# Kernel tuning notes

Hardware: AMD Instinct MI355X
Metric: run time of the kernel (lower is better)

## Reference

```python
import jax, jax.numpy as jnp
import numpy as np

B, T, E, D, A = 32, 2048, 1024, 1024, 1024
SHARPENING = 1.0


def setup_inputs() -> dict:
    key = jax.random.key(0)
    ks = jax.random.split(key, 8)
    s = 0.02
    return {
        "enc_out": jax.random.normal(ks[0], (B, T, E), jnp.float32),
        "x_lens": jax.random.randint(ks[1], (B,), 1, T + 1, jnp.int32),
        "dec_out": jax.random.normal(ks[2], (B, 1, D), jnp.float32),
        "att_weights_step": jax.random.uniform(ks[3], (B, T), jnp.float32),
        "W_enc": jax.random.normal(ks[4], (E, A), jnp.float32) * s,
        "b_enc": jnp.zeros((A,), jnp.float32),
        "W_dec": jax.random.normal(ks[5], (D, A), jnp.float32) * s,
        "v": jax.random.normal(ks[6], (A,), jnp.float32) * s,
    }


def reference(enc_out, x_lens, dec_out, att_weights_step, W_enc, b_enc, W_dec, v):
    # content (Bahdanau additive) attention
    # energy[b,t] = v . tanh(W_enc enc[b,t] + b_enc + W_dec dec[b])
    enc_proj = jnp.einsum("bte,ea->bta", enc_out, W_enc) + b_enc  # [B,T,A]
    dec_proj = jnp.einsum("bod,da->boa", dec_out, W_dec)          # [B,1,A]
    energy = jnp.einsum("bta,a->bt", jnp.tanh(enc_proj + dec_proj), v)  # [B,T]
    # original multiplies energy by a 0/1 length mask (NOT -inf masking)
    mask = (jnp.arange(T)[None, :] < x_lens[:, None]).astype(energy.dtype)
    energy = energy * mask * SHARPENING
    att = jax.nn.softmax(energy, axis=-1)  # [B,T]
    context_vec = jnp.einsum("bte,bt->be", enc_out, att)[:, None, :]  # [B,1,E]
    return context_vec, att
```

## Files before the change

### kernel.cpp

```cpp
#include <hip/hip_runtime.h>
#include <hip/hip_bf16.h>
#include <stdint.h>


typedef __bf16 bf16;
typedef __bf16 bf16x8 __attribute__((ext_vector_type(8)));
typedef __bf16 bf16x4 __attribute__((ext_vector_type(4)));
typedef float floatx4 __attribute__((ext_vector_type(4)));

#define T_DIM 2048
#define B_DIM 32
#define K_DIM 1024
#define N_DIM 1024
#define M_DIM (B_DIM * T_DIM)
#define ENC_ELEMS ((size_t)M_DIM * K_DIM)

__device__ __forceinline__ void async_copy16(const bf16* g, bf16* l) {
    __builtin_amdgcn_global_load_lds(
        (const __attribute__((address_space(1))) void*)g,
        (__attribute__((address_space(3))) void*)l, 16, 0, 0);
}

__device__ __forceinline__ float fast_tanh(float x) {
    float ax = fabsf(x);
    float e  = __expf(ax + ax);
    float t  = 1.f - 2.f / (e + 1.f);
    return copysignf(t, x);
}

__global__ __launch_bounds__(256) void cvt_enc(const float* __restrict__ in,
                                               bf16* __restrict__ out) {
    size_t i = ((size_t)blockIdx.x * 256 + threadIdx.x) * 8;
    const size_t stride = (size_t)gridDim.x * 256 * 8;
    for (; i < ENC_ELEMS; i += stride) {
        float4 f0 = *(const float4*)(in + i);
        float4 f1 = *(const float4*)(in + i + 4);
        bf16x8 w;
        w[0] = (bf16)f0.x; w[1] = (bf16)f0.y; w[2] = (bf16)f0.z; w[3] = (bf16)f0.w;
        w[4] = (bf16)f1.x; w[5] = (bf16)f1.y; w[6] = (bf16)f1.z; w[7] = (bf16)f1.w;
        *(bf16x8*)(out + i) = w;
    }
}

__global__ __launch_bounds__(256) void transpose_wenc(
        const float* __restrict__ W, bf16* __restrict__ WT) {
    __shared__ bf16 tile[64][65];
    const int e0 = blockIdx.x * 64, a0 = blockIdx.y * 64;
    const int c = threadIdx.x & 63, r0 = threadIdx.x >> 6;
#pragma unroll
    for (int p = 0; p < 16; ++p) {
        int r = p * 4 + r0;
        tile[r][c] = (bf16)W[(size_t)(e0 + r) * 1024 + a0 + c];
    }
    __syncthreads();
#pragma unroll
    for (int p = 0; p < 16; ++p) {
        int r = p * 4 + r0;
        WT[(size_t)(a0 + r) * 1024 + e0 + c] = tile[c][r];
    }
}

__global__ __launch_bounds__(256) void decproj_kernel(
        const float* __restrict__ dec, const float* __restrict__ Wdec,
        const float* __restrict__ benc, float* __restrict__ dproj) {
    const int bg = blockIdx.x;
    const int y  = blockIdx.y;
    const int a  = y * 256 + threadIdx.x;
    __shared__ float sdec[8][1024];
    for (int i = threadIdx.x; i < 8 * 1024; i += 256)
        sdec[i >> 10][i & 1023] = dec[bg * 8192 + i];
    __syncthreads();
    float acc[8];
    const float be = benc[a];
#pragma unroll
    for (int b = 0; b < 8; ++b) acc[b] = be;
    for (int d = 0; d < 1024; ++d) {
        const float w = Wdec[(size_t)d * 1024 + a];
#pragma unroll
        for (int b = 0; b < 8; ++b) acc[b] += sdec[b][d] * w;
    }
#pragma unroll
    for (int b = 0; b < 8; ++b) dproj[(bg * 8 + b) * 1024 + a] = acc[b];
}


#define HT 8192

#define BARRIER()  asm volatile("s_barrier" ::: "memory")
#define VMCNT(n)   asm volatile("s_waitcnt vmcnt(" #n ")" ::: "memory")

#define STAGE_A(kt, h) {                                                       \
    const bf16* g_ = encb + (size_t)(m0 + (h)*128 + wave*8 + (lane>>3)) * 1024 \
                     + (kt)*64 + srccol;                                       \
    bf16* l_ = As + ((((kt)&1)*2 + (h)) * HT) + wave * 512;                    \
    async_copy16(g_, l_);                                                      \
    async_copy16(g_ + (size_t)64*1024, l_ + 4096);                             \
}
#define STAGE_B(kt, h) {                                                       \
    const bf16* g_ = WT + (size_t)(n0 + (h)*128 + wave*8 + (lane>>3)) * 1024   \
                     + (kt)*64 + srccol;                                       \
    bf16* l_ = Bs + ((((kt)&1)*2 + (h)) * HT) + wave * 512;                    \
    async_copy16(g_, l_);                                                      \
    async_copy16(g_ + (size_t)64*1024, l_ + 4096);                             \
}

#define PHASE(tt, qm, qn, RA, STAGECODE, WAITCODE) {                           \
    const bf16* Ah_ = As + (((tt)&1)*2 + (qm)) * HT;                           \
    const bf16* Bh_ = Bs + (((tt)&1)*2 + (qn)) * HT;                           \
    if (RA) {                                                                  \
      _Pragma("unroll") for (int mf_ = 0; mf_ < 4; ++mf_) {                    \
        afr[mf_][0] = *(const bf16x8*)(Ah_ + (wm*64 + mf_*16 + lo)*64 + swz0); \
        afr[mf_][1] = *(const bf16x8*)(Ah_ + (wm*64 + mf_*16 + lo)*64 + swz1); \
      }                                                                        \
    }                                                                          \
    _Pragma("unroll") for (int nf_ = 0; nf_ < 2; ++nf_) {                      \
      bfr[nf_][0] = *(const bf16x8*)(Bh_ + (wn*32 + nf_*16 + lo)*64 + swz0);   \
      bfr[nf_][1] = *(const bf16x8*)(Bh_ + (wn*32 + nf_*16 + lo)*64 + swz1);   \
    }                                                                          \
    STAGECODE;                                                                 \
    BARRIER();                                                                 \
    __builtin_amdgcn_s_setprio(1);                                             \
    _Pragma("unroll") for (int kk_ = 0; kk_ < 2; ++kk_)                        \
      _Pragma("unroll") for (int mf_ = 0; mf_ < 4; ++mf_)                      \
        _Pragma("unroll") for (int nf_ = 0; nf_ < 2; ++nf_)                    \
          acc[qm][qn][mf_][nf_] = __builtin_amdgcn_mfma_f32_16x16x32_bf16(     \
              afr[mf_][kk_], bfr[nf_][kk_], acc[qm][qn][mf_][nf_], 0, 0, 0);   \
    __builtin_amdgcn_s_setprio(0);                                             \
    WAITCODE;                                                                  \
    BARRIER();                                                                 \
}

__global__ __launch_bounds__(512, 2) void energy_gemm_8ph(
        const bf16* __restrict__ encb, const bf16* __restrict__ WT,
        const float* __restrict__ dproj, const float* __restrict__ v,
        float* __restrict__ part) {
    __shared__ __align__(16) bf16 As[4 * HT];
    __shared__ __align__(16) bf16 Bs[4 * HT];

    const int tid  = threadIdx.x;
    const int lane = tid & 63;
    const int wave = tid >> 6;
    const int wm   = wave >> 2;
    const int wn   = wave & 3;
    const int lo   = lane & 15;
    const int hi   = lane >> 4;

    const int L = blockIdx.x;
    const int xcd  = L & 7;
    const int slot = L >> 3;
    const int m_tile  = xcd * 32 + (slot >> 2);
    const int n_chunk = slot & 3;
    const int m0 = m_tile * 256;
    const int n0 = n_chunk * 256;
    const int b  = m0 >> 11;

    const int srccol = (((lane & 7) ^ (lane >> 3)) << 3);
    const int swz0 = ((hi)     ^ (lo & 7)) << 3;
    const int swz1 = ((4 | hi) ^ (lo & 7)) << 3;

    floatx4 acc[2][2][4][2];
#pragma unroll
    for (int a_ = 0; a_ < 2; ++a_)
#pragma unroll
      for (int b_ = 0; b_ < 2; ++b_)
#pragma unroll
        for (int c_ = 0; c_ < 4; ++c_)
#pragma unroll
          for (int d_ = 0; d_ < 2; ++d_)
            acc[a_][b_][c_][d_] = (floatx4){0.f, 0.f, 0.f, 0.f};

    bf16x8 afr[4][2], bfr[2][2];

    STAGE_A(0, 0); STAGE_B(0, 0); STAGE_A(0, 1); STAGE_B(0, 1);
    STAGE_A(1, 0); STAGE_B(1, 0);
    VMCNT(4);
    BARRIER();

#pragma unroll 1
    for (int i = 0; i < 7; ++i) {
        const int t0 = 2 * i, t1 = 2 * i + 1, t2 = 2 * i + 2, t3 = 2 * i + 3;
        PHASE(t0, 0, 0, 1, { STAGE_A(t1, 1); }, {});
        PHASE(t0, 0, 1, 0, { STAGE_B(t1, 1); }, {});
        PHASE(t0, 1, 0, 1, { STAGE_A(t2, 0); }, {});
        PHASE(t0, 1, 1, 0, { STAGE_B(t2, 0); }, { VMCNT(4); });
        PHASE(t1, 0, 0, 1, { STAGE_A(t2, 1); }, {});
        PHASE(t1, 0, 1, 0, { STAGE_B(t2, 1); }, {});
        PHASE(t1, 1, 0, 1, { STAGE_A(t3, 0); }, {});
        PHASE(t1, 1, 1, 0, { STAGE_B(t3, 0); }, { VMCNT(4); });
    }
    PHASE(14, 0, 0, 1, { STAGE_A(15, 1); }, {});
    PHASE(14, 0, 1, 0, { STAGE_B(15, 1); }, {});
    PHASE(14, 1, 0, 1, {}, {});
    PHASE(14, 1, 1, 0, {}, { VMCNT(0); });
    PHASE(15, 0, 0, 1, {}, {});
    PHASE(15, 0, 1, 0, {}, {});
    PHASE(15, 1, 0, 1, {}, {});
    PHASE(15, 1, 1, 0, {}, {});

    float* esump = (float*)As;

    float vv[2][2], dp[2][2];
#pragma unroll
    for (int qn = 0; qn < 2; ++qn)
#pragma unroll
      for (int nf = 0; nf < 2; ++nf) {
        int col = n0 + qn * 128 + wn * 32 + nf * 16 + lo;
        vv[qn][nf] = v[col];
        dp[qn][nf] = dproj[b * 1024 + col];
      }
#pragma unroll
    for (int qm = 0; qm < 2; ++qm)
#pragma unroll
      for (int mf = 0; mf < 4; ++mf)
#pragma unroll
        for (int r = 0; r < 4; ++r) {
          float s = 0.f;
#pragma unroll
          for (int qn = 0; qn < 2; ++qn)
#pragma unroll
            for (int nf = 0; nf < 2; ++nf)
              s += vv[qn][nf] * fast_tanh(acc[qm][qn][mf][nf][r] + dp[qn][nf]);
          s += __shfl_xor(s, 1);
          s += __shfl_xor(s, 2);
          s += __shfl_xor(s, 4);
          s += __shfl_xor(s, 8);
          if (lo == 0)
            esump[wn * 256 + qm * 128 + wm * 64 + mf * 16 + hi * 4 + r] = s;
        }
    __syncthreads();
    if (tid < 256) {
        float s = esump[tid] + esump[256 + tid] + esump[512 + tid] + esump[768 + tid];
        part[(size_t)n_chunk * M_DIM + m0 + tid] = s;
    }
}

__global__ __launch_bounds__(256) void energy_gemm_f32(
        const float* __restrict__ enc, const bf16* __restrict__ WT,
        const float* __restrict__ dproj, const float* __restrict__ v,
        float* __restrict__ part) {
    __shared__ __align__(16) bf16 As[128 * 32];
    __shared__ __align__(16) bf16 Bs[128 * 32];
    __shared__ float esum[128];

    const int tid  = threadIdx.x;
    const int lane = tid & 63;
    const int wave = tid >> 6;
    const int wy = wave >> 1, wx = wave & 1;
    const int L = blockIdx.x;
    const int xcd  = L & 7;
    const int slot = L >> 3;
    const int m_tile = xcd * 64 + (slot >> 3);
    const int n_chunk = slot & 7;
    const int m0 = m_tile * 128;
    const int n0 = n_chunk * 128;
    const int b  = m0 >> 11;

    if (tid < 128) esum[tid] = 0.f;

    floatx4 acc[4][4];
#pragma unroll
    for (int i = 0; i < 4; ++i)
#pragma unroll
        for (int j = 0; j < 4; ++j) acc[i][j] = (floatx4){0.f, 0.f, 0.f, 0.f};

    const int sr = tid >> 2;
    const int sc = (tid & 3) * 8;
    const float* gA = enc + (size_t)(m0 + sr) * 1024 + sc;
    const bf16*  gB = WT  + (size_t)(n0 + sr) * 1024 + sc;
    bf16* lA = As + sr * 32 + sc;
    bf16* lB = Bs + sr * 32 + sc;

    for (int k0 = 0; k0 < K_DIM; k0 += 32) {
        __syncthreads();
#pragma unroll
        for (int rep = 0; rep < 2; ++rep) {
            const float4* p = (const float4*)(gA + (size_t)rep * 64 * 1024 + k0);
            float4 f0 = p[0], f1 = p[1];
            bf16x8 w;
            w[0] = (bf16)f0.x; w[1] = (bf16)f0.y; w[2] = (bf16)f0.z; w[3] = (bf16)f0.w;
            w[4] = (bf16)f1.x; w[5] = (bf16)f1.y; w[6] = (bf16)f1.z; w[7] = (bf16)f1.w;
            *(bf16x8*)(lA + rep * 64 * 32) = w;
            *(bf16x8*)(lB + rep * 64 * 32) =
                *(const bf16x8*)(gB + (size_t)rep * 64 * 1024 + k0);
        }
        __syncthreads();

        bf16x8 af[4], bfrg[4];
#pragma unroll
        for (int i = 0; i < 4; ++i)
            af[i] = *(const bf16x8*)(As + (wy * 64 + i * 16 + (lane & 15)) * 32 + (lane >> 4) * 8);
#pragma unroll
        for (int i = 0; i < 4; ++i)
            bfrg[i] = *(const bf16x8*)(Bs + (wx * 64 + i * 16 + (lane & 15)) * 32 + (lane >> 4) * 8);
#pragma unroll
        for (int mi = 0; mi < 4; ++mi)
#pragma unroll
            for (int ni = 0; ni < 4; ++ni)
                acc[mi][ni] = __builtin_amdgcn_mfma_f32_16x16x32_bf16(
                    af[mi], bfrg[ni], acc[mi][ni], 0, 0, 0);
    }
    __syncthreads();

    float vv[4], dp[4];
#pragma unroll
    for (int ni = 0; ni < 4; ++ni) {
        int col = n0 + wx * 64 + ni * 16 + (lane & 15);
        vv[ni] = v[col];
        dp[ni] = dproj[b * 1024 + col];
    }
#pragma unroll
    for (int mi = 0; mi < 4; ++mi) {
#pragma unroll
        for (int r = 0; r < 4; ++r) {
            float s = 0.f;
#pragma unroll
            for (int ni = 0; ni < 4; ++ni)
                s += vv[ni] * fast_tanh(acc[mi][ni][r] + dp[ni]);
            s += __shfl_xor(s, 1);
            s += __shfl_xor(s, 2);
            s += __shfl_xor(s, 4);
            s += __shfl_xor(s, 8);
            if ((lane & 15) == 0) {
                int row = wy * 64 + mi * 16 + (lane >> 4) * 4 + r;
                atomicAdd(&esum[row], s);
            }
        }
    }
    __syncthreads();
    if (tid < 128) part[(size_t)n_chunk * M_DIM + m0 + tid] = esum[tid];
}

__global__ __launch_bounds__(256) void softmax_kernel(
        const float* __restrict__ part, const int* __restrict__ xlens,
        float* __restrict__ att, int nc) {
    const int b = blockIdx.x, tid = threadIdx.x;
    const int len = xlens[b];
    float e[8];
    float mx = -3.4e38f;
#pragma unroll
    for (int i = 0; i < 8; ++i) {
        const int t = tid + i * 256;
        float s = 0.f;
#pragma unroll 4
        for (int c = 0; c < nc; ++c) s += part[(size_t)c * M_DIM + b * 2048 + t];
        e[i] = (t < len) ? s : 0.f;
        mx = fmaxf(mx, e[i]);
    }
#pragma unroll
    for (int off = 1; off < 64; off <<= 1) mx = fmaxf(mx, __shfl_xor(mx, off));
    __shared__ float sr1[4], sr2[4];
    if ((tid & 63) == 0) sr1[tid >> 6] = mx;
    __syncthreads();
    mx = fmaxf(fmaxf(sr1[0], sr1[1]), fmaxf(sr1[2], sr1[3]));
    float sum = 0.f;
#pragma unroll
    for (int i = 0; i < 8; ++i) { e[i] = __expf(e[i] - mx); sum += e[i]; }
#pragma unroll
    for (int off = 1; off < 64; off <<= 1) sum += __shfl_xor(sum, off);
    if ((tid & 63) == 0) sr2[tid >> 6] = sum;
    __syncthreads();
    sum = sr2[0] + sr2[1] + sr2[2] + sr2[3];
    const float inv = 1.f / sum;
#pragma unroll
    for (int i = 0; i < 8; ++i)
        att[b * 2048 + tid + i * 256] = e[i] * inv;
}

__global__ __launch_bounds__(256) void context_part_kernel(
        const bf16* __restrict__ encb, const float* __restrict__ att,
        float* __restrict__ ctxpart) {
    const int b = blockIdx.x, chunk = blockIdx.y, tid = threadIdx.x;
    const int t0 = chunk * 128;
    __shared__ float satt[128];
    if (tid < 128) satt[tid] = att[b * 2048 + t0 + tid];
    __syncthreads();
    const bf16* base = encb + ((size_t)b * 2048 + t0) * 1024 + tid * 4;
    float a0 = 0.f, a1 = 0.f, a2 = 0.f, a3 = 0.f;
#pragma unroll 4
    for (int t = 0; t < 128; ++t) {
        bf16x4 ev = *(const bf16x4*)(base + (size_t)t * 1024);
        float w = satt[t];
        a0 += w * (float)ev[0]; a1 += w * (float)ev[1];
        a2 += w * (float)ev[2]; a3 += w * (float)ev[3];
    }
    float* o = ctxpart + ((size_t)b * 16 + chunk) * 1024 + tid * 4;
    o[0] = a0; o[1] = a1; o[2] = a2; o[3] = a3;
}

__global__ __launch_bounds__(256) void context_reduce_kernel(
        const float* __restrict__ ctxpart, float* __restrict__ out_ctx) {
    const int i = blockIdx.x * 256 + threadIdx.x;
    const int b = i >> 10, e = i & 1023;
    const float* p = ctxpart + (size_t)b * 16 * 1024 + e;
    float s = 0.f;
#pragma unroll
    for (int c = 0; c < 16; ++c) s += p[c * 1024];
    out_ctx[i] = s;
}

__global__ __launch_bounds__(256) void context_kernel_f32(
        const float* __restrict__ enc, const float* __restrict__ att,
        float* __restrict__ ctx) {
    const int b = blockIdx.x, t0 = blockIdx.y * 128, tid = threadIdx.x;
    __shared__ float satt[128];
    if (tid < 128) satt[tid] = att[b * 2048 + t0 + tid];
    __syncthreads();
    const float* base = enc + ((size_t)b * 2048 + t0) * 1024 + tid * 4;
    float a0 = 0.f, a1 = 0.f, a2 = 0.f, a3 = 0.f;
    for (int t = 0; t < 128; ++t) {
        float4 ev = *(const float4*)(base + (size_t)t * 1024);
        float w = satt[t];
        a0 += w * ev.x; a1 += w * ev.y; a2 += w * ev.z; a3 += w * ev.w;
    }
    float* o = ctx + b * 1024 + tid * 4;
    atomicAdd(o + 0, a0); atomicAdd(o + 1, a1);
    atomicAdd(o + 2, a2); atomicAdd(o + 3, a3);
}

extern "C" void kernel_launch(void* const* d_in, const int* in_sizes, int n_in,
                              void* d_out, int out_size, void* d_ws, size_t ws_size,
                              hipStream_t stream) {
    const float* enc   = (const float*)d_in[0];
    const int*   xlens = (const int*)d_in[1];
    const float* dec   = (const float*)d_in[2];
    const float* Wenc  = (const float*)d_in[4];
    const float* benc  = (const float*)d_in[5];
    const float* Wdec  = (const float*)d_in[6];
    const float* v     = (const float*)d_in[7];

    float* out_ctx = (float*)d_out;
    float* out_att = out_ctx + B_DIM * K_DIM;

    char* ws = (char*)d_ws;
    float* dproj   = (float*)ws;
    bf16*  WT      = (bf16*)(ws + (128u << 10));
    float* part    = (float*)(ws + (128u << 10) + (2u << 20));
    bf16*  encb    = (bf16*)(ws + (128u << 10) + (4u << 20));
    float* ctxpart = (float*)(ws + (128u << 10) + (4u << 20) + (ENC_ELEMS * 2));
    const size_t need = (128u << 10) + (4u << 20) + ENC_ELEMS * 2 + (2u << 21);

    transpose_wenc<<<dim3(16, 16), 256, 0, stream>>>(Wenc, WT);
    decproj_kernel<<<dim3(4, 4), 256, 0, stream>>>(dec, Wdec, benc, dproj);

    if (ws_size >= need) {
        cvt_enc<<<2048, 256, 0, stream>>>(enc, encb);
        energy_gemm_8ph<<<1024, 512, 0, stream>>>(encb, WT, dproj, v, part);
        softmax_kernel<<<B_DIM, 256, 0, stream>>>(part, xlens, out_att, 4);
        context_part_kernel<<<dim3(B_DIM, 16), 256, 0, stream>>>(encb, out_att, ctxpart);
        context_reduce_kernel<<<B_DIM * K_DIM / 256, 256, 0, stream>>>(ctxpart, out_ctx);
    } else {
        hipMemsetAsync(out_ctx, 0, B_DIM * K_DIM * sizeof(float), stream);
        energy_gemm_f32<<<4096, 256, 0, stream>>>(enc, WT, dproj, v, part);
        softmax_kernel<<<B_DIM, 256, 0, stream>>>(part, xlens, out_att, 8);
        context_kernel_f32<<<dim3(B_DIM, 16), 256, 0, stream>>>(enc, out_att, out_ctx);
    }
}
```

Measured before the change: 671.6 us.

## Make energy GEMM persistent over four M tiles and split decproj reduction

```diff
diff --git a/kernel.cpp b/kernel.cpp
--- a/kernel.cpp
+++ b/kernel.cpp
@@ -64,23 +64,33 @@
         const float* __restrict__ dec, const float* __restrict__ Wdec,
         const float* __restrict__ benc, float* __restrict__ dproj) {
     const int bg = blockIdx.x;
-    const int y  = blockIdx.y;
-    const int a  = y * 256 + threadIdx.x;
+    const int a0 = blockIdx.y * 64;
+    const int al = threadIdx.x & 63;
+    const int dq = threadIdx.x >> 6;
+    const int a  = a0 + al;
     __shared__ float sdec[8][1024];
-    for (int i = threadIdx.x; i < 8 * 1024; i += 256)
+    for (int i = threadIdx.x; i < 8192; i += 256)
         sdec[i >> 10][i & 1023] = dec[bg * 8192 + i];
     __syncthreads();
     float acc[8];
-    const float be = benc[a];
-#pragma unroll
-    for (int b = 0; b < 8; ++b) acc[b] = be;
-    for (int d = 0; d < 1024; ++d) {
+#pragma unroll
+    for (int b = 0; b < 8; ++b) acc[b] = 0.f;
+    for (int d = dq * 256; d < dq * 256 + 256; ++d) {
         const float w = Wdec[(size_t)d * 1024 + a];
 #pragma unroll
         for (int b = 0; b < 8; ++b) acc[b] += sdec[b][d] * w;
     }
-#pragma unroll
-    for (int b = 0; b < 8; ++b) dproj[(bg * 8 + b) * 1024 + a] = acc[b];
+    __shared__ float red[4][8][64];
+#pragma unroll
+    for (int b = 0; b < 8; ++b) red[dq][b][al] = acc[b];
+    __syncthreads();
+    if (dq == 0) {
+        const float be = benc[a];
+#pragma unroll
+        for (int b = 0; b < 8; ++b)
+            dproj[(bg * 8 + b) * 1024 + a] =
+                be + red[0][b][al] + red[1][b][al] + red[2][b][al] + red[3][b][al];
+    }
 }
 
 
@@ -89,24 +99,25 @@
 #define BARRIER()  asm volatile("s_barrier" ::: "memory")
 #define VMCNT(n)   asm volatile("s_waitcnt vmcnt(" #n ")" ::: "memory")
 
-#define STAGE_A(kt, h) {                                                       \
-    const bf16* g_ = encb + (size_t)(m0 + (h)*128 + wave*8 + (lane>>3)) * 1024 \
-                     + (kt)*64 + srccol;                                       \
-    bf16* l_ = As + ((((kt)&1)*2 + (h)) * HT) + wave * 512;                    \
+#define STAGE_A(gt, h) {                                                       \
+    const bf16* g_ = encb + (size_t)(m0 + ((gt) >> 4) * 256 + (h) * 128        \
+                     + wave * 8 + (lane >> 3)) * 1024 + ((gt) & 15) * 64       \
+                     + srccol;                                                 \
+    bf16* l_ = As + ((((gt) & 1) * 2 + (h)) * HT) + wave * 512;                \
     async_copy16(g_, l_);                                                      \
-    async_copy16(g_ + (size_t)64*1024, l_ + 4096);                             \
-}
-#define STAGE_B(kt, h) {                                                       \
-    const bf16* g_ = WT + (size_t)(n0 + (h)*128 + wave*8 + (lane>>3)) * 1024   \
-                     + (kt)*64 + srccol;                                       \
-    bf16* l_ = Bs + ((((kt)&1)*2 + (h)) * HT) + wave * 512;                    \
+    async_copy16(g_ + (size_t)64 * 1024, l_ + 4096);                           \
+}
+#define STAGE_B(gt, h) {                                                       \
+    const bf16* g_ = WT + (size_t)(n0 + (h) * 128 + wave * 8 + (lane >> 3))    \
+                     * 1024 + ((gt) & 15) * 64 + srccol;                       \
+    bf16* l_ = Bs + ((((gt) & 1) * 2 + (h)) * HT) + wave * 512;                \
     async_copy16(g_, l_);                                                      \
-    async_copy16(g_ + (size_t)64*1024, l_ + 4096);                             \
+    async_copy16(g_ + (size_t)64 * 1024, l_ + 4096);                           \
 }
 
 #define PHASE(tt, qm, qn, RA, STAGECODE, WAITCODE) {                           \
-    const bf16* Ah_ = As + (((tt)&1)*2 + (qm)) * HT;                           \
-    const bf16* Bh_ = Bs + (((tt)&1)*2 + (qn)) * HT;                           \
+    const bf16* Ah_ = As + (((tt) & 1) * 2 + (qm)) * HT;                       \
+    const bf16* Bh_ = Bs + (((tt) & 1) * 2 + (qn)) * HT;                       \
     if (RA) {                                                                  \
       _Pragma("unroll") for (int mf_ = 0; mf_ < 4; ++mf_) {                    \
         afr[mf_][0] = *(const bf16x8*)(Ah_ + (wm*64 + mf_*16 + lo)*64 + swz0); \
@@ -136,6 +147,8 @@
         float* __restrict__ part) {
     __shared__ __align__(16) bf16 As[4 * HT];
     __shared__ __align__(16) bf16 Bs[4 * HT];
+    __shared__ float esum[4 * 256];
+    __shared__ float esumAll[4 * 256];
 
     const int tid  = threadIdx.x;
     const int lane = tid & 63;
@@ -148,11 +161,11 @@
     const int L = blockIdx.x;
     const int xcd  = L & 7;
     const int slot = L >> 3;
-    const int m_tile  = xcd * 32 + (slot >> 2);
+    const int m_group = xcd * 8 + (slot >> 2);
     const int n_chunk = slot & 3;
-    const int m0 = m_tile * 256;
+    const int m0 = m_group * 1024;
     const int n0 = n_chunk * 256;
-    const int b  = m0 >> 11;
+    const int b  = m_group >> 1;
 
     const int srccol = (((lane & 7) ^ (lane >> 3)) << 3);
     const int swz0 = ((hi)     ^ (lo & 7)) << 3;
@@ -170,34 +183,6 @@
             acc[a_][b_][c_][d_] = (floatx4){0.f, 0.f, 0.f, 0.f};
 
     bf16x8 afr[4][2], bfr[2][2];
-
-    STAGE_A(0, 0); STAGE_B(0, 0); STAGE_A(0, 1); STAGE_B(0, 1);
-    STAGE_A(1, 0); STAGE_B(1, 0);
-    VMCNT(4);
-    BARRIER();
-
-#pragma unroll 1
-    for (int i = 0; i < 7; ++i) {
-        const int t0 = 2 * i, t1 = 2 * i + 1, t2 = 2 * i + 2, t3 = 2 * i + 3;
-        PHASE(t0, 0, 0, 1, { STAGE_A(t1, 1); }, {});
-        PHASE(t0, 0, 1, 0, { STAGE_B(t1, 1); }, {});
-        PHASE(t0, 1, 0, 1, { STAGE_A(t2, 0); }, {});
-        PHASE(t0, 1, 1, 0, { STAGE_B(t2, 0); }, { VMCNT(4); });
-        PHASE(t1, 0, 0, 1, { STAGE_A(t2, 1); }, {});
-        PHASE(t1, 0, 1, 0, { STAGE_B(t2, 1); }, {});
-        PHASE(t1, 1, 0, 1, { STAGE_A(t3, 0); }, {});
-        PHASE(t1, 1, 1, 0, { STAGE_B(t3, 0); }, { VMCNT(4); });
-    }
-    PHASE(14, 0, 0, 1, { STAGE_A(15, 1); }, {});
-    PHASE(14, 0, 1, 0, { STAGE_B(15, 1); }, {});
-    PHASE(14, 1, 0, 1, {}, {});
-    PHASE(14, 1, 1, 0, {}, { VMCNT(0); });
-    PHASE(15, 0, 0, 1, {}, {});
-    PHASE(15, 0, 1, 0, {}, {});
-    PHASE(15, 1, 0, 1, {}, {});
-    PHASE(15, 1, 1, 0, {}, {});
-
-    float* esump = (float*)As;
 
     float vv[2][2], dp[2][2];
 #pragma unroll
@@ -208,29 +193,77 @@
         vv[qn][nf] = v[col];
         dp[qn][nf] = dproj[b * 1024 + col];
       }
-#pragma unroll
-    for (int qm = 0; qm < 2; ++qm)
-#pragma unroll
-      for (int mf = 0; mf < 4; ++mf)
-#pragma unroll
-        for (int r = 0; r < 4; ++r) {
-          float s = 0.f;
-#pragma unroll
-          for (int qn = 0; qn < 2; ++qn)
-#pragma unroll
-            for (int nf = 0; nf < 2; ++nf)
-              s += vv[qn][nf] * fast_tanh(acc[qm][qn][mf][nf][r] + dp[qn][nf]);
-          s += __shfl_xor(s, 1);
-          s += __shfl_xor(s, 2);
-          s += __shfl_xor(s, 4);
-          s += __shfl_xor(s, 8);
-          if (lo == 0)
-            esump[wn * 256 + qm * 128 + wm * 64 + mf * 16 + hi * 4 + r] = s;
+    VMCNT(0);
+
+    STAGE_A(0, 0); STAGE_B(0, 0); STAGE_A(0, 1); STAGE_B(0, 1);
+    STAGE_A(1, 0); STAGE_B(1, 0);
+    VMCNT(4);
+    BARRIER();
+
+    for (int pass = 0; pass < 4; ++pass) {
+        const int iiEnd = (pass == 3) ? 7 : 8;
+#pragma unroll 1
+        for (int ii = 0; ii < iiEnd; ++ii) {
+            const int gi = pass * 8 + ii;
+            const int t0 = 2 * gi, t1 = t0 + 1, t2 = t0 + 2, t3 = t0 + 3;
+            PHASE(t0, 0, 0, 1, { STAGE_A(t1, 1); }, {});
+            PHASE(t0, 0, 1, 0, { STAGE_B(t1, 1); }, {});
+            PHASE(t0, 1, 0, 1, { STAGE_A(t2, 0); }, {});
+            PHASE(t0, 1, 1, 0, { STAGE_B(t2, 0); }, { VMCNT(4); });
+            PHASE(t1, 0, 0, 1, { STAGE_A(t2, 1); }, {});
+            PHASE(t1, 0, 1, 0, { STAGE_B(t2, 1); }, {});
+            PHASE(t1, 1, 0, 1, { STAGE_A(t3, 0); }, {});
+            PHASE(t1, 1, 1, 0, { STAGE_B(t3, 0); }, { VMCNT(4); });
         }
-    __syncthreads();
-    if (tid < 256) {
-        float s = esump[tid] + esump[256 + tid] + esump[512 + tid] + esump[768 + tid];
-        part[(size_t)n_chunk * M_DIM + m0 + tid] = s;
+        if (pass == 3) {
+            PHASE(62, 0, 0, 1, { STAGE_A(63, 1); }, {});
+            PHASE(62, 0, 1, 0, { STAGE_B(63, 1); }, {});
+            PHASE(62, 1, 0, 1, {}, {});
+            PHASE(62, 1, 1, 0, {}, { VMCNT(0); });
+            PHASE(63, 0, 0, 1, {}, {});
+            PHASE(63, 0, 1, 0, {}, {});
+            PHASE(63, 1, 0, 1, {}, {});
+            PHASE(63, 1, 1, 0, {}, {});
+        }
+
+#pragma unroll
+        for (int qm = 0; qm < 2; ++qm)
+#pragma unroll
+          for (int mf = 0; mf < 4; ++mf)
+#pragma unroll
+            for (int r = 0; r < 4; ++r) {
+              float s = 0.f;
+#pragma unroll
+              for (int qn = 0; qn < 2; ++qn)
+#pragma unroll
+                for (int nf = 0; nf < 2; ++nf)
+                  s += vv[qn][nf] * fast_tanh(acc[qm][qn][mf][nf][r] + dp[qn][nf]);
+              s += __shfl_xor(s, 1);
+              s += __shfl_xor(s, 2);
+              s += __shfl_xor(s, 4);
+              s += __shfl_xor(s, 8);
+              if (lo == 0)
+                esum[wn * 256 + qm * 128 + wm * 64 + mf * 16 + hi * 4 + r] = s;
+            }
+        __syncthreads();
+        if (tid < 256)
+            esumAll[pass * 256 + tid] =
+                esum[tid] + esum[256 + tid] + esum[512 + tid] + esum[768 + tid];
+#pragma unroll
+        for (int a_ = 0; a_ < 2; ++a_)
+#pragma unroll
+          for (int b_ = 0; b_ < 2; ++b_)
+#pragma unroll
+            for (int c_ = 0; c_ < 4; ++c_)
+#pragma unroll
+              for (int d_ = 0; d_ < 2; ++d_)
+                acc[a_][b_][c_][d_] = (floatx4){0.f, 0.f, 0.f, 0.f};
+    }
+    __syncthreads();
+    {
+        const size_t base = (size_t)n_chunk * M_DIM + (size_t)m0;
+        part[base + tid]       = esumAll[tid];
+        part[base + 512 + tid] = esumAll[512 + tid];
     }
 }
 
@@ -440,11 +473,11 @@
     const size_t need = (128u << 10) + (4u << 20) + ENC_ELEMS * 2 + (2u << 21);
 
     transpose_wenc<<<dim3(16, 16), 256, 0, stream>>>(Wenc, WT);
-    decproj_kernel<<<dim3(4, 4), 256, 0, stream>>>(dec, Wdec, benc, dproj);
+    decproj_kernel<<<dim3(4, 16), 256, 0, stream>>>(dec, Wdec, benc, dproj);
 
     if (ws_size >= need) {
         cvt_enc<<<2048, 256, 0, stream>>>(enc, encb);
-        energy_gemm_8ph<<<1024, 512, 0, stream>>>(encb, WT, dproj, v, part);
+        energy_gemm_8ph<<<256, 512, 0, stream>>>(encb, WT, dproj, v, part);
         softmax_kernel<<<B_DIM, 256, 0, stream>>>(part, xlens, out_att, 4);
         context_part_kernel<<<dim3(B_DIM, 16), 256, 0, stream>>>(encb, out_att, ctxpart);
         context_reduce_kernel<<<B_DIM * K_DIM / 256, 256, 0, stream>>>(ctxpart, out_ctx);
```

New measurement: 616.5 us. 8.2% less time.

## Split decproj reduction across waves and pin GEMM scheduling with sched barriers

Applied to the files above, without the earlier changes.

```diff
diff --git a/kernel.cpp b/kernel.cpp
--- a/kernel.cpp
+++ b/kernel.cpp
@@ -64,30 +64,41 @@
         const float* __restrict__ dec, const float* __restrict__ Wdec,
         const float* __restrict__ benc, float* __restrict__ dproj) {
     const int bg = blockIdx.x;
-    const int y  = blockIdx.y;
-    const int a  = y * 256 + threadIdx.x;
+    const int a0 = blockIdx.y * 64;
+    const int al = threadIdx.x & 63;
+    const int dq = threadIdx.x >> 6;
+    const int a  = a0 + al;
     __shared__ float sdec[8][1024];
-    for (int i = threadIdx.x; i < 8 * 1024; i += 256)
+    for (int i = threadIdx.x; i < 8192; i += 256)
         sdec[i >> 10][i & 1023] = dec[bg * 8192 + i];
     __syncthreads();
     float acc[8];
-    const float be = benc[a];
-#pragma unroll
-    for (int b = 0; b < 8; ++b) acc[b] = be;
-    for (int d = 0; d < 1024; ++d) {
+#pragma unroll
+    for (int b = 0; b < 8; ++b) acc[b] = 0.f;
+    for (int d = dq * 256; d < dq * 256 + 256; ++d) {
         const float w = Wdec[(size_t)d * 1024 + a];
 #pragma unroll
         for (int b = 0; b < 8; ++b) acc[b] += sdec[b][d] * w;
     }
-#pragma unroll
-    for (int b = 0; b < 8; ++b) dproj[(bg * 8 + b) * 1024 + a] = acc[b];
+    __shared__ float red[4][8][64];
+#pragma unroll
+    for (int b = 0; b < 8; ++b) red[dq][b][al] = acc[b];
+    __syncthreads();
+    if (dq == 0) {
+        const float be = benc[a];
+#pragma unroll
+        for (int b = 0; b < 8; ++b)
+            dproj[(bg * 8 + b) * 1024 + a] =
+                be + red[0][b][al] + red[1][b][al] + red[2][b][al] + red[3][b][al];
+    }
 }
 
 
 #define HT 8192
 
-#define BARRIER()  asm volatile("s_barrier" ::: "memory")
-#define VMCNT(n)   asm volatile("s_waitcnt vmcnt(" #n ")" ::: "memory")
+#define BARRIER()  __builtin_amdgcn_s_barrier()
+#define SCHEDB()   __builtin_amdgcn_sched_barrier(0)
+#define VMCNT(n)   asm volatile("s_waitcnt vmcnt(" #n ")")
 
 #define STAGE_A(kt, h) {                                                       \
     const bf16* g_ = encb + (size_t)(m0 + (h)*128 + wave*8 + (lane>>3)) * 1024 \
@@ -105,8 +116,8 @@
 }
 
 #define PHASE(tt, qm, qn, RA, STAGECODE, WAITCODE) {                           \
-    const bf16* Ah_ = As + (((tt)&1)*2 + (qm)) * HT;                           \
-    const bf16* Bh_ = Bs + (((tt)&1)*2 + (qn)) * HT;                           \
+    const bf16* Ah_ = As + (((tt) & 1) * 2 + (qm)) * HT;                       \
+    const bf16* Bh_ = Bs + (((tt) & 1) * 2 + (qn)) * HT;                       \
     if (RA) {                                                                  \
       _Pragma("unroll") for (int mf_ = 0; mf_ < 4; ++mf_) {                    \
         afr[mf_][0] = *(const bf16x8*)(Ah_ + (wm*64 + mf_*16 + lo)*64 + swz0); \
@@ -118,7 +129,9 @@
       bfr[nf_][1] = *(const bf16x8*)(Bh_ + (wn*32 + nf_*16 + lo)*64 + swz1);   \
     }                                                                          \
     STAGECODE;                                                                 \
+    SCHEDB();                                                                  \
     BARRIER();                                                                 \
+    SCHEDB();                                                                  \
     __builtin_amdgcn_s_setprio(1);                                             \
     _Pragma("unroll") for (int kk_ = 0; kk_ < 2; ++kk_)                        \
       _Pragma("unroll") for (int mf_ = 0; mf_ < 4; ++mf_)                      \
@@ -126,8 +139,11 @@
           acc[qm][qn][mf_][nf_] = __builtin_amdgcn_mfma_f32_16x16x32_bf16(     \
               afr[mf_][kk_], bfr[nf_][kk_], acc[qm][qn][mf_][nf_], 0, 0, 0);   \
     __builtin_amdgcn_s_setprio(0);                                             \
+    SCHEDB();                                                                  \
     WAITCODE;                                                                  \
+    SCHEDB();                                                                  \
     BARRIER();                                                                 \
+    SCHEDB();                                                                  \
 }
 
 __global__ __launch_bounds__(512, 2) void energy_gemm_8ph(
@@ -136,6 +152,7 @@
         float* __restrict__ part) {
     __shared__ __align__(16) bf16 As[4 * HT];
     __shared__ __align__(16) bf16 Bs[4 * HT];
+    __shared__ float esum[4 * 256];
 
     const int tid  = threadIdx.x;
     const int lane = tid & 63;
@@ -171,14 +188,30 @@
 
     bf16x8 afr[4][2], bfr[2][2];
 
+    float vv[2][2], dp[2][2];
+#pragma unroll
+    for (int qn = 0; qn < 2; ++qn)
+#pragma unroll
+      for (int nf = 0; nf < 2; ++nf) {
+        int col = n0 + qn * 128 + wn * 32 + nf * 16 + lo;
+        vv[qn][nf] = v[col];
+        dp[qn][nf] = dproj[b * 1024 + col];
+      }
+    SCHEDB();
+    VMCNT(0);
+    SCHEDB();
+
     STAGE_A(0, 0); STAGE_B(0, 0); STAGE_A(0, 1); STAGE_B(0, 1);
     STAGE_A(1, 0); STAGE_B(1, 0);
+    SCHEDB();
     VMCNT(4);
+    SCHEDB();
     BARRIER();
+    SCHEDB();
 
 #pragma unroll 1
     for (int i = 0; i < 7; ++i) {
-        const int t0 = 2 * i, t1 = 2 * i + 1, t2 = 2 * i + 2, t3 = 2 * i + 3;
+        const int t0 = 2 * i, t1 = t0 + 1, t2 = t0 + 2, t3 = t0 + 3;
         PHASE(t0, 0, 0, 1, { STAGE_A(t1, 1); }, {});
         PHASE(t0, 0, 1, 0, { STAGE_B(t1, 1); }, {});
         PHASE(t0, 1, 0, 1, { STAGE_A(t2, 0); }, {});
@@ -197,17 +230,6 @@
     PHASE(15, 1, 0, 1, {}, {});
     PHASE(15, 1, 1, 0, {}, {});
 
-    float* esump = (float*)As;
-
-    float vv[2][2], dp[2][2];
-#pragma unroll
-    for (int qn = 0; qn < 2; ++qn)
-#pragma unroll
-      for (int nf = 0; nf < 2; ++nf) {
-        int col = n0 + qn * 128 + wn * 32 + nf * 16 + lo;
-        vv[qn][nf] = v[col];
-        dp[qn][nf] = dproj[b * 1024 + col];
-      }
 #pragma unroll
     for (int qm = 0; qm < 2; ++qm)
 #pragma unroll
@@ -225,13 +247,12 @@
           s += __shfl_xor(s, 4);
           s += __shfl_xor(s, 8);
           if (lo == 0)
-            esump[wn * 256 + qm * 128 + wm * 64 + mf * 16 + hi * 4 + r] = s;
+            esum[wn * 256 + qm * 128 + wm * 64 + mf * 16 + hi * 4 + r] = s;
         }
     __syncthreads();
-    if (tid < 256) {
-        float s = esump[tid] + esump[256 + tid] + esump[512 + tid] + esump[768 + tid];
-        part[(size_t)n_chunk * M_DIM + m0 + tid] = s;
-    }
+    if (tid < 256)
+        part[(size_t)n_chunk * M_DIM + m0 + tid] =
+            esum[tid] + esum[256 + tid] + esum[512 + tid] + esum[768 + tid];
 }
 
 __global__ __launch_bounds__(256) void energy_gemm_f32(
@@ -440,7 +461,7 @@
     const size_t need = (128u << 10) + (4u << 20) + ENC_ELEMS * 2 + (2u << 21);
 
     transpose_wenc<<<dim3(16, 16), 256, 0, stream>>>(Wenc, WT);
-    decproj_kernel<<<dim3(4, 4), 256, 0, stream>>>(dec, Wdec, benc, dproj);
+    decproj_kernel<<<dim3(4, 16), 256, 0, stream>>>(dec, Wdec, benc, dproj);
 
     if (ws_size >= need) {
         cvt_enc<<<2048, 256, 0, stream>>>(enc, encb);
```

New measurement: 621.2 us. 7.5% less time.
